# Kernel tuning notes

Measured on AMD Instinct MI355X. Metric: run time of the kernel, lower is better.

Reference implementation:

```python
import jax, jax.numpy as jnp
import numpy as np


def setup_inputs() -> dict:
    key = jax.random.key(0)
    ks = jax.random.split(key, 6)
    B, deep_C, shallow_C, H, W = 4, 256, 64, 64, 64
    qk_C = shallow_C // 4  # 16
    deep = jax.random.normal(ks[0], (B, deep_C, H, W), dtype=jnp.float32)
    shallow = jax.random.normal(ks[1], (B, shallow_C, H, W), dtype=jnp.float32)
    # 1x1 conv weights (out_ch, in_ch), fan-in scaled like torch conv init
    Wq = jax.random.normal(ks[2], (qk_C, shallow_C), dtype=jnp.float32) / np.sqrt(shallow_C)
    bq = jnp.zeros((qk_C,), dtype=jnp.float32)
    Wk = jax.random.normal(ks[3], (qk_C, shallow_C), dtype=jnp.float32) / np.sqrt(shallow_C)
    bk = jnp.zeros((qk_C,), dtype=jnp.float32)
    gamma = jnp.ones((1,), dtype=jnp.float32)
    return {"deep": deep, "shallow": shallow, "Wq": Wq, "bq": bq, "Wk": Wk, "bk": bk, "gamma": gamma}


def reference(deep, shallow, Wq, bq, Wk, bk, gamma):
    B, deep_C, H, W = deep.shape
    N = H * W
    # 1x1 convs == per-pixel linear maps
    q = jnp.einsum('oc,bchw->bohw', Wq, shallow) + bq[None, :, None, None]  # [B,qk_C,H,W]
    k = jnp.einsum('oc,bchw->bohw', Wk, shallow) + bk[None, :, None, None]
    qk_C = q.shape[1]
    q = q.reshape(B, qk_C, N)  # [B,qk_C,N]
    k = k.reshape(B, qk_C, N)
    # energy[b, i, j] = q_i . k_j  (NO 1/sqrt(d) scaling, faithful to original)
    energy = jnp.einsum('bci,bcj->bij', q, k)  # [B,N,N]
    attention = jax.nn.softmax(energy, axis=-1)  # [B,N,N]
    v = deep.reshape(B, deep_C, N)  # value taken directly from deep features
    # out = V @ attention^T : out[b,c,m] = sum_n v[b,c,n] * attention[b,m,n]
    out = jnp.einsum('bcn,bmn->bcm', v, attention)
    out = out.reshape(B, deep_C, H, W)
    return gamma * out + deep
```

## Files before the change

kernel.cpp:

```cpp
#include <hip/hip_runtime.h>
#include <hip/hip_bf16.h>
#include <stdint.h>

#define LOG2E 1.44269504088896340736f

typedef _Float16 f16x8  __attribute__((ext_vector_type(8)));
typedef __bf16   bf16x8 __attribute__((ext_vector_type(8)));
typedef float    f32x16 __attribute__((ext_vector_type(16)));

__device__ __forceinline__ uint32_t pack_f16_rn(float a, float b) {
    uint16_t ua = __builtin_bit_cast(uint16_t, (_Float16)a);
    uint16_t ub = __builtin_bit_cast(uint16_t, (_Float16)b);
    return (uint32_t)ua | ((uint32_t)ub << 16);
}
__device__ __forceinline__ uint32_t pack_bf2(float a, float b) {
    uint16_t ua = __builtin_bit_cast(uint16_t, (__bf16)a);
    uint16_t ub = __builtin_bit_cast(uint16_t, (__bf16)b);
    return (uint32_t)ua | ((uint32_t)ub << 16);
}

__global__ void __launch_bounds__(256) prepass(
    const float* __restrict__ deep, const float* __restrict__ shallow,
    const float* __restrict__ Wq, const float* __restrict__ bq,
    const float* __restrict__ Wk, const float* __restrict__ bk,
    uint16_t* __restrict__ Vb, uint16_t* __restrict__ Qb,
    uint16_t* __restrict__ Kb3) {
    __shared__ uint16_t tile[32 * 516];
    const int blk = blockIdx.x;
    if (blk < 128) {
        const bool doQ = (blk < 64);
        int gid = (doQ ? blk : blk - 64) * 256 + threadIdx.x;
        int b = gid >> 12;
        int n = gid & 4095;
        const float* sp = shallow + (size_t)b * 64 * 4096 + n;
        const float* W  = doQ ? Wq : Wk;
        const float* bi = doQ ? bq : bk;
        float v[16];
#pragma unroll
        for (int o = 0; o < 16; ++o) v[o] = bi[o];
#pragma unroll 4
        for (int c = 0; c < 64; ++c) {
            float s = sp[(size_t)c * 4096];
#pragma unroll
            for (int o = 0; o < 16; ++o) v[o] = fmaf(W[o * 64 + c], s, v[o]);
        }
        if (doQ) {
            uint16_t* qr = Qb + (size_t)gid * 16;
            *(uint4*)(qr)     = make_uint4(pack_f16_rn(v[0]*LOG2E,  v[1]*LOG2E),
                                           pack_f16_rn(v[2]*LOG2E,  v[3]*LOG2E),
                                           pack_f16_rn(v[4]*LOG2E,  v[5]*LOG2E),
                                           pack_f16_rn(v[6]*LOG2E,  v[7]*LOG2E));
            *(uint4*)(qr + 8) = make_uint4(pack_f16_rn(v[8]*LOG2E,  v[9]*LOG2E),
                                           pack_f16_rn(v[10]*LOG2E, v[11]*LOG2E),
                                           pack_f16_rn(v[12]*LOG2E, v[13]*LOG2E),
                                           pack_f16_rn(v[14]*LOG2E, v[15]*LOG2E));
        } else {
            uint16_t* kr = Kb3 + (size_t)(b * 128 + (n >> 5)) * 512 + (size_t)(n & 31) * 8;
            *(uint4*)(kr)       = make_uint4(pack_f16_rn(v[0],  v[1]),  pack_f16_rn(v[2],  v[3]),
                                             pack_f16_rn(v[4],  v[5]),  pack_f16_rn(v[6],  v[7]));
            *(uint4*)(kr + 256) = make_uint4(pack_f16_rn(v[8],  v[9]),  pack_f16_rn(v[10], v[11]),
                                             pack_f16_rn(v[12], v[13]), pack_f16_rn(v[14], v[15]));
        }
    } else {
        const int vb_id = blk - 128;
        const int b  = vb_id >> 6;
        const int ct = (vb_id >> 3) & 7;
        const int kseg = vb_id & 7;
        const int tid = threadIdx.x;
        const int k4 = tid & 63;
        const int cb = tid >> 6;
        const size_t dbase = ((size_t)(b * 256 + ct * 32) * 4096) + kseg * 512;
#pragma unroll
        for (int p = 0; p < 16; ++p) {
            int c   = (p & 7) * 4 + cb;
            int key = (p >> 3) * 256 + k4 * 4;
            float4 f = *(const float4*)(deep + dbase + (size_t)c * 4096 + key);
            *(uint2*)&tile[c * 516 + key] =
                make_uint2(pack_bf2(f.x, f.y), pack_bf2(f.z, f.w));
        }
        __syncthreads();
        const int c   = tid & 31;
        const int h1  = (tid >> 5) & 1;
        const int kb0 = tid >> 6;
#pragma unroll
        for (int p2 = 0; p2 < 8; ++p2) {
            int kb = p2 * 4 + kb0;
            const uint16_t* t = &tile[c * 516 + kb * 16 + h1 * 8];
            uint2 lo = *(const uint2*)(t);
            uint2 hi = *(const uint2*)(t + 4);
            size_t u = (((size_t)((b * 8 + ct) * 256 + kseg * 32 + kb) * 2) + h1) * 32 + c;
            ((uint4*)Vb)[u] = make_uint4(lo.x, lo.y, hi.x, hi.y);
        }
    }
}

__global__ void __launch_bounds__(1024, 4) attn_main(
    const uint16_t* __restrict__ Qb, const uint16_t* __restrict__ Kb3,
    const uint16_t* __restrict__ Vb, const float* __restrict__ deep,
    const float* __restrict__ gamma, float* __restrict__ out) {
    const int lane = threadIdx.x & 63;
    const int w    = threadIdx.x >> 6;
    const int ks   = w & 7;
    const int sel  = w >> 3;
    const int col  = lane & 31;
    const int h1   = lane >> 5;

    const int bid = blockIdx.x;
    const int xcd = bid & 7;
    const int b   = xcd >> 1;
    const int qt  = ((bid >> 3) << 1) + (xcd & 1);
    const int n0q = qt * 64;

    __shared__ uint4 Pl[2][2][16][2][32];
    __shared__ float Lf[2][16][32];

    const uint16_t* qrow = Qb + ((size_t)(b * 4096 + n0q + sel * 32 + col)) * 16;
    uint4 ubq = *(const uint4*)(qrow + h1 * 8);

    const uint16_t* kbase = Kb3 + (size_t)b * 65536 + (size_t)ks * 512
                                + (size_t)lane * 8;
    const uint16_t* vlane = Vb + (size_t)(b * 8 + ks) * 131072
                               + (size_t)sel * 4096
                               + (size_t)h1 * 256 + (size_t)col * 8;

    f32x16 acc0 = {0,0,0,0,0,0,0,0,0,0,0,0,0,0,0,0};
    f32x16 acc1 = {0,0,0,0,0,0,0,0,0,0,0,0,0,0,0,0};
    float lacc = 0.0f;
    uint4 uk;

    auto qk_softmax = [&](int s) {
        const int pr = s & 1;
        f16x8 ak = __builtin_bit_cast(f16x8, uk);
        f16x8 bq = __builtin_bit_cast(f16x8, ubq);
        f32x16 e = {0,0,0,0,0,0,0,0,0,0,0,0,0,0,0,0};
        e = __builtin_amdgcn_mfma_f32_32x32x16_f16(ak, bq, e, 0, 0, 0);
        const int sn = (s < 15) ? s + 1 : s;
        uk = *(const uint4*)(kbase + (size_t)sn * 4096);
        float p[16];
#pragma unroll
        for (int r = 0; r < 16; ++r) p[r] = exp2f(e[r]);
        float t0 = (p[0] + p[1]) + (p[2] + p[3]);
        float t1 = (p[4] + p[5]) + (p[6] + p[7]);
        float t2 = (p[8] + p[9]) + (p[10] + p[11]);
        float t3 = (p[12] + p[13]) + (p[14] + p[15]);
        lacc += (t0 + t1) + (t2 + t3);
        uint32_t pk0 = pack_bf2(p[0],  p[1]),  pk1 = pack_bf2(p[2],  p[3]);
        uint32_t pk2 = pack_bf2(p[4],  p[5]),  pk3 = pack_bf2(p[6],  p[7]);
        uint32_t pk4 = pack_bf2(p[8],  p[9]),  pk5 = pack_bf2(p[10], p[11]);
        uint32_t pk6 = pack_bf2(p[12], p[13]), pk7 = pack_bf2(p[14], p[15]);
        ((uint2*)&Pl[pr][sel][2 * ks    ][0][col])[h1] = make_uint2(pk0, pk1);
        ((uint2*)&Pl[pr][sel][2 * ks    ][1][col])[h1] = make_uint2(pk2, pk3);
        ((uint2*)&Pl[pr][sel][2 * ks + 1][0][col])[h1] = make_uint2(pk4, pk5);
        ((uint2*)&Pl[pr][sel][2 * ks + 1][1][col])[h1] = make_uint2(pk6, pk7);
    };

#define LBAR()                                                      \
    {                                                               \
        asm volatile("s_waitcnt lgkmcnt(0)" ::: "memory");          \
        __builtin_amdgcn_s_barrier();                               \
    }

    uk = *(const uint4*)(kbase);
    qk_softmax(0);
    LBAR();

#pragma unroll 2
    for (int ss = 0; ss < 16; ++ss) {
        const int par = ss & 1;
        uint4 vr[8];
        const uint16_t* vss = vlane + (size_t)ss * 8192;
#pragma unroll
        for (int j = 0; j < 8; ++j) vr[j] = *(const uint4*)(vss + j * 512);

        if (ss < 15) qk_softmax(ss + 1);

        __builtin_amdgcn_s_setprio(1);
#pragma unroll
        for (int j = 0; j < 8; ++j) {
            const int f = sel * 8 + j;
            uint4 pb0 = Pl[par][0][f][h1][col];
            uint4 pb1 = Pl[par][1][f][h1][col];
            bf16x8 av = __builtin_bit_cast(bf16x8, vr[j]);
            acc0 = __builtin_amdgcn_mfma_f32_32x32x16_bf16(
                av, __builtin_bit_cast(bf16x8, pb0), acc0, 0, 0, 0);
            acc1 = __builtin_amdgcn_mfma_f32_32x32x16_bf16(
                av, __builtin_bit_cast(bf16x8, pb1), acc1, 0, 0, 0);
        }
        __builtin_amdgcn_s_setprio(0);
        LBAR();
    }

    Lf[sel][ks * 2 + h1][col] = lacc;
    float* Ex = (float*)&Pl[0][0][0][0][0];
    float* myEx = Ex + ((size_t)w * 64 + lane) * 16;
    if (w < 8) {
#pragma unroll
        for (int r = 0; r < 16; ++r) myEx[r] = acc1[r];
    } else {
#pragma unroll
        for (int r = 0; r < 16; ++r) myEx[r] = acc0[r];
    }
    LBAR();
    const float* pEx = Ex + ((size_t)(w ^ 8) * 64 + lane) * 16;
    float l = 0.0f;
#pragma unroll
    for (int j = 0; j < 16; ++j) l += Lf[sel][j][col];
    const float gr = gamma[0] / l;

    if (w < 8) {
#pragma unroll
        for (int r = 0; r < 16; ++r) {
            float a = acc0[r] + pEx[r];
            const int crow = (r & 3) + 8 * (r >> 2) + 4 * h1;
            size_t i0 = (size_t)(b * 256 + ks * 32 + crow) * 4096 + n0q + col;
            out[i0] = fmaf(gr, a, deep[i0]);
        }
    } else {
#pragma unroll
        for (int r = 0; r < 16; ++r) {
            float a = acc1[r] + pEx[r];
            const int crow = (r & 3) + 8 * (r >> 2) + 4 * h1;
            size_t i1 = (size_t)(b * 256 + ks * 32 + crow) * 4096 + n0q + 32 + col;
            out[i1] = fmaf(gr, a, deep[i1]);
        }
    }
#undef LBAR
}

extern "C" void kernel_launch(void* const* d_in, const int* in_sizes, int n_in,
                              void* d_out, int out_size, void* d_ws, size_t ws_size,
                              hipStream_t stream) {
    const float* deep    = (const float*)d_in[0];
    const float* shallow = (const float*)d_in[1];
    const float* Wq      = (const float*)d_in[2];
    const float* bq      = (const float*)d_in[3];
    const float* Wk      = (const float*)d_in[4];
    const float* bk      = (const float*)d_in[5];
    const float* gamma   = (const float*)d_in[6];
    float* out = (float*)d_out;

    uint16_t* Vb  = (uint16_t*)d_ws;
    uint16_t* Qb  = (uint16_t*)((char*)d_ws + (size_t)8 * 1024 * 1024);
    uint16_t* Kb3 = (uint16_t*)((char*)d_ws + (size_t)9 * 1024 * 1024);

    hipLaunchKernelGGL(prepass, dim3(384), dim3(256), 0, stream,
                       deep, shallow, Wq, bq, Wk, bk, Vb, Qb, Kb3);
    hipLaunchKernelGGL(attn_main, dim3(256), dim3(1024), 0, stream,
                       Qb, Kb3, Vb, deep, gamma, out);
}
```

Before: 62.31 us.

## Halve query tile per block to 32 and double grid to 512 blocks

Each attention block now handles 32 queries instead of 64, so the grid doubles to 512 blocks with one accumulator per wave. Only the first half of the waves computes QK^T and softmax; all waves then split the PV reduction over keys and combine their partials through LDS. The goal is more blocks for occupancy and lower register pressure per wave, with launch bounds raised to match. In exchange every block re-reads the full V and K for half as many queries, doubling V traffic, and half the waves sit idle during the softmax stage.

```diff
diff --git a/kernel.cpp b/kernel.cpp
--- a/kernel.cpp
+++ b/kernel.cpp
@@ -94,7 +94,7 @@
     }
 }
 
-__global__ void __launch_bounds__(1024, 4) attn_main(
+__global__ void __launch_bounds__(1024, 8) attn_main(
     const uint16_t* __restrict__ Qb, const uint16_t* __restrict__ Kb3,
     const uint16_t* __restrict__ Vb, const float* __restrict__ deep,
     const float* __restrict__ gamma, float* __restrict__ out) {
@@ -109,24 +109,26 @@
     const int xcd = bid & 7;
     const int b   = xcd >> 1;
     const int qt  = ((bid >> 3) << 1) + (xcd & 1);
-    const int n0q = qt * 64;
-
-    __shared__ uint4 Pl[2][2][16][2][32];
-    __shared__ float Lf[2][16][32];
-
-    const uint16_t* qrow = Qb + ((size_t)(b * 4096 + n0q + sel * 32 + col)) * 16;
-    uint4 ubq = *(const uint4*)(qrow + h1 * 8);
-
-    const uint16_t* kbase = Kb3 + (size_t)b * 65536 + (size_t)ks * 512
-                                + (size_t)lane * 8;
+    const int n0q = qt * 32;
+
+    __shared__ uint4 Pl[2][16][2][32];
+    __shared__ float Lf[16][32];
+
+    uint4 ubq;
+    const uint16_t* kbase = nullptr;
+    uint4 uk;
+    if (sel == 0) {
+        const uint16_t* qrow = Qb + ((size_t)(b * 4096 + n0q + col)) * 16;
+        ubq = *(const uint4*)(qrow + h1 * 8);
+        kbase = Kb3 + (size_t)b * 65536 + (size_t)ks * 512 + (size_t)lane * 8;
+        uk = *(const uint4*)(kbase);
+    }
     const uint16_t* vlane = Vb + (size_t)(b * 8 + ks) * 131072
                                + (size_t)sel * 4096
                                + (size_t)h1 * 256 + (size_t)col * 8;
 
-    f32x16 acc0 = {0,0,0,0,0,0,0,0,0,0,0,0,0,0,0,0};
-    f32x16 acc1 = {0,0,0,0,0,0,0,0,0,0,0,0,0,0,0,0};
+    f32x16 acc = {0,0,0,0,0,0,0,0,0,0,0,0,0,0,0,0};
     float lacc = 0.0f;
-    uint4 uk;
 
     auto qk_softmax = [&](int s) {
         const int pr = s & 1;
@@ -148,10 +150,10 @@
         uint32_t pk2 = pack_bf2(p[4],  p[5]),  pk3 = pack_bf2(p[6],  p[7]);
         uint32_t pk4 = pack_bf2(p[8],  p[9]),  pk5 = pack_bf2(p[10], p[11]);
         uint32_t pk6 = pack_bf2(p[12], p[13]), pk7 = pack_bf2(p[14], p[15]);
-        ((uint2*)&Pl[pr][sel][2 * ks    ][0][col])[h1] = make_uint2(pk0, pk1);
-        ((uint2*)&Pl[pr][sel][2 * ks    ][1][col])[h1] = make_uint2(pk2, pk3);
-        ((uint2*)&Pl[pr][sel][2 * ks + 1][0][col])[h1] = make_uint2(pk4, pk5);
-        ((uint2*)&Pl[pr][sel][2 * ks + 1][1][col])[h1] = make_uint2(pk6, pk7);
+        ((uint2*)&Pl[pr][2 * ks    ][0][col])[h1] = make_uint2(pk0, pk1);
+        ((uint2*)&Pl[pr][2 * ks    ][1][col])[h1] = make_uint2(pk2, pk3);
+        ((uint2*)&Pl[pr][2 * ks + 1][0][col])[h1] = make_uint2(pk4, pk5);
+        ((uint2*)&Pl[pr][2 * ks + 1][1][col])[h1] = make_uint2(pk6, pk7);
     };
 
 #define LBAR()                                                      \
@@ -160,68 +162,49 @@
         __builtin_amdgcn_s_barrier();                               \
     }
 
-    uk = *(const uint4*)(kbase);
-    qk_softmax(0);
+    if (sel == 0) qk_softmax(0);
     LBAR();
 
-#pragma unroll 2
     for (int ss = 0; ss < 16; ++ss) {
         const int par = ss & 1;
+        if (sel == 0 && ss < 15) qk_softmax(ss + 1);
         uint4 vr[8];
         const uint16_t* vss = vlane + (size_t)ss * 8192;
 #pragma unroll
         for (int j = 0; j < 8; ++j) vr[j] = *(const uint4*)(vss + j * 512);
-
-        if (ss < 15) qk_softmax(ss + 1);
-
         __builtin_amdgcn_s_setprio(1);
 #pragma unroll
         for (int j = 0; j < 8; ++j) {
             const int f = sel * 8 + j;
-            uint4 pb0 = Pl[par][0][f][h1][col];
-            uint4 pb1 = Pl[par][1][f][h1][col];
-            bf16x8 av = __builtin_bit_cast(bf16x8, vr[j]);
-            acc0 = __builtin_amdgcn_mfma_f32_32x32x16_bf16(
-                av, __builtin_bit_cast(bf16x8, pb0), acc0, 0, 0, 0);
-            acc1 = __builtin_amdgcn_mfma_f32_32x32x16_bf16(
-                av, __builtin_bit_cast(bf16x8, pb1), acc1, 0, 0, 0);
+            uint4 pb = Pl[par][f][h1][col];
+            acc = __builtin_amdgcn_mfma_f32_32x32x16_bf16(
+                __builtin_bit_cast(bf16x8, vr[j]),
+                __builtin_bit_cast(bf16x8, pb), acc, 0, 0, 0);
         }
         __builtin_amdgcn_s_setprio(0);
         LBAR();
     }
 
-    Lf[sel][ks * 2 + h1][col] = lacc;
-    float* Ex = (float*)&Pl[0][0][0][0][0];
-    float* myEx = Ex + ((size_t)w * 64 + lane) * 16;
+    if (sel == 0) Lf[ks * 2 + h1][col] = lacc;
+    float* Ex = (float*)&Pl[0][0][0][0];
+    if (w >= 8) {
+        float* myEx = Ex + ((size_t)(w - 8) * 64 + lane) * 16;
+#pragma unroll
+        for (int r = 0; r < 16; ++r) myEx[r] = acc[r];
+    }
+    LBAR();
     if (w < 8) {
-#pragma unroll
-        for (int r = 0; r < 16; ++r) myEx[r] = acc1[r];
-    } else {
-#pragma unroll
-        for (int r = 0; r < 16; ++r) myEx[r] = acc0[r];
-    }
-    LBAR();
-    const float* pEx = Ex + ((size_t)(w ^ 8) * 64 + lane) * 16;
-    float l = 0.0f;
-#pragma unroll
-    for (int j = 0; j < 16; ++j) l += Lf[sel][j][col];
-    const float gr = gamma[0] / l;
-
-    if (w < 8) {
+        const float* pEx = Ex + ((size_t)w * 64 + lane) * 16;
+        float l = 0.0f;
+#pragma unroll
+        for (int j = 0; j < 16; ++j) l += Lf[j][col];
+        const float gr = gamma[0] / l;
 #pragma unroll
         for (int r = 0; r < 16; ++r) {
-            float a = acc0[r] + pEx[r];
+            float a = acc[r] + pEx[r];
             const int crow = (r & 3) + 8 * (r >> 2) + 4 * h1;
             size_t i0 = (size_t)(b * 256 + ks * 32 + crow) * 4096 + n0q + col;
             out[i0] = fmaf(gr, a, deep[i0]);
-        }
-    } else {
-#pragma unroll
-        for (int r = 0; r < 16; ++r) {
-            float a = acc1[r] + pEx[r];
-            const int crow = (r & 3) + 8 * (r >> 2) + 4 * h1;
-            size_t i1 = (size_t)(b * 256 + ks * 32 + crow) * 4096 + n0q + 32 + col;
-            out[i1] = fmaf(gr, a, deep[i1]);
         }
     }
 #undef LBAR
@@ -245,6 +228,6 @@
 
     hipLaunchKernelGGL(prepass, dim3(384), dim3(256), 0, stream,
                        deep, shallow, Wq, bq, Wk, bk, Vb, Qb, Kb3);
-    hipLaunchKernelGGL(attn_main, dim3(256), dim3(1024), 0, stream,
+    hipLaunchKernelGGL(attn_main, dim3(512), dim3(1024), 0, stream,
                        Qb, Kb3, Vb, deep, gamma, out);
 }
```

Result: slower. 91.30 us (+46.5%).
